# Kernel tuning notes

Measured on AMD Instinct MI355X. Metric: run time of the kernel, lower is better.

The kernel has to match this reference:

```python
import jax, jax.numpy as jnp
import numpy as np

B = 1048576
IN, H = 16, 12


def _xavier(key, shape):
    fan_out, fan_in = shape
    lim = jnp.sqrt(6.0 / (fan_in + fan_out))
    return jax.random.uniform(key, shape, jnp.float32, -lim, lim)


def _lstm_cell_zero_state(x, W_ih, b_ih, b_hh):
    # PyTorch LSTMCell with h0=c0=0: h0 @ W_hh.T == 0, so W_hh drops out of
    # the forward math (its gradient is exactly zero); b_hh still contributes.
    gates = x @ W_ih.T + b_ih + b_hh          # [B, 4H]
    i, f, g, o = jnp.split(gates, 4, axis=-1)  # PyTorch gate order: i,f,g,o
    c = jax.nn.sigmoid(i) * jnp.tanh(g)        # f*c0 == 0
    h = jax.nn.sigmoid(o) * jnp.tanh(c)
    return h


def setup_inputs() -> dict:
    key = jax.random.key(0)
    ks = jax.random.split(key, 9)
    x = jax.random.normal(ks[0], (B, IN), jnp.float32)
    d = {"x": x}
    specs = [("1", IN), ("2", H), ("m", H), ("d", H)]
    for idx, (tag, in_dim) in enumerate(specs):
        kw, kb = jax.random.split(ks[idx + 1])
        d[f"W_ih{tag}"] = _xavier(kw, (4 * H, in_dim))
        kb1, kb2 = jax.random.split(kb)
        lim = 1.0 / np.sqrt(H)
        d[f"b_ih{tag}"] = jax.random.uniform(kb1, (4 * H,), jnp.float32, -lim, lim)
        d[f"b_hh{tag}"] = jax.random.uniform(kb2, (4 * H,), jnp.float32, -lim, lim)
    return d


def reference(x, W_ih1, b_ih1, b_hh1, W_ih2, b_ih2, b_hh2,
              W_ihm, b_ihm, b_hhm, W_ihd, b_ihd, b_hhd):
    h1 = jax.nn.relu(_lstm_cell_zero_state(x, W_ih1, b_ih1, b_hh1))
    h2 = jax.nn.selu(_lstm_cell_zero_state(h1, W_ih2, b_ih2, b_hh2))
    m = jnp.tanh(_lstm_cell_zero_state(h2, W_ihm, b_ihm, b_hhm))
    dv = jnp.tanh(_lstm_cell_zero_state(h2, W_ihd, b_ihd, b_hhd))
    return jnp.concatenate([m, dv], axis=0)  # [2B, H]
```

## Files before the change

### kernel.cpp

```cpp
#include <hip/hip_runtime.h>

#define L2E 1.4426950408889634f

typedef float v2f __attribute__((ext_vector_type(2)));

__device__ __forceinline__ v2f exp2v(v2f a) {
    v2f r; r.x = __builtin_amdgcn_exp2f(a.x); r.y = __builtin_amdgcn_exp2f(a.y); return r;
}
__device__ __forceinline__ v2f rcpv(v2f a) {
    v2f r; r.x = __builtin_amdgcn_rcpf(a.x); r.y = __builtin_amdgcn_rcpf(a.y); return r;
}
__device__ __forceinline__ v2f fmav(v2f a, v2f b, v2f c) {
    return __builtin_elementwise_fma(a, b, c);
}
__device__ __forceinline__ v2f tanh_pade(v2f xv) {
    v2f x2 = xv * xv;
    v2f num = xv * (945.0f + x2 * (105.0f + x2));
    v2f den = 945.0f + x2 * (420.0f + 15.0f * x2);
    return num * rcpv(den);
}

__global__ void prep_kernel(
    const float* __restrict__ W1, const float* __restrict__ bi1, const float* __restrict__ bh1,
    const float* __restrict__ W2, const float* __restrict__ bi2, const float* __restrict__ bh2,
    const float* __restrict__ Wm, const float* __restrict__ bim, const float* __restrict__ bhm,
    const float* __restrict__ Wd, const float* __restrict__ bid, const float* __restrict__ bhd,
    float* __restrict__ ws)
{
    const float* Ws[4]  = {W1, W2, Wm, Wd};
    const float* bis[4] = {bi1, bi2, bim, bid};
    const float* bhs[4] = {bh1, bh2, bhm, bhd};
    const int   Ks[4]   = {16, 12, 12, 12};
    const int   wOff[4] = {0, 576, 1008, 1440};
    const int   goff[3] = {0, 24, 36};
    const float gsc[3]  = {-L2E, -2.0f * L2E, -L2E};

    int tid = threadIdx.x + blockIdx.x * blockDim.x;
    int nth = blockDim.x * gridDim.x;
    for (int c = 0; c < 4; ++c) {
        int K = Ks[c];
        int n = 3 * 6 * K * 2;
        for (int t = tid; t < n; t += nth) {
            int e  = t & 1;
            int u  = t >> 1;
            int k  = u % K;
            int g  = (u / K) % 3;
            int jp = u / (3 * K);
            int row = goff[g] + 2 * jp + e;
            ws[wOff[c] + t] = gsc[g] * Ws[c][row * K + k];
        }
        for (int t = tid; t < 36; t += nth) {
            int e  = t & 1;
            int u  = t >> 1;
            int g  = u % 3;
            int jp = u / 3;
            int row = goff[g] + 2 * jp + e;
            ws[1872 + c * 36 + t] = gsc[g] * (bis[c][row] + bhs[c][row]);
        }
    }
}

template <int K>
__device__ __forceinline__ void cell_core(const float* __restrict__ wsW,
                                          const float* __restrict__ wsB,
                                          const v2f* xs, v2f h[6])
{
#pragma unroll
    for (int jp = 0; jp < 6; ++jp) {
        const v2f* w  = reinterpret_cast<const v2f*>(wsW) + jp * 3 * K;
        const v2f* bp = reinterpret_cast<const v2f*>(wsB) + jp * 3;
        v2f ai = bp[0], ag = bp[1], ao = bp[2];
#pragma unroll
        for (int k = 0; k < K; ++k) {
            ai = fmav(w[k],         xs[k], ai);
            ag = fmav(w[K + k],     xs[k], ag);
            ao = fmav(w[2 * K + k], xs[k], ao);
        }
        v2f ei = exp2v(ai);
        v2f tg = exp2v(ag);
        v2f eo = exp2v(ao);
        v2f r_ig = rcpv((1.0f + ei) * (1.0f + tg));
        v2f c    = (1.0f - tg) * r_ig;
        v2f c2   = c * c;
        v2f num  = c * (945.0f + c2 * (105.0f + c2));
        v2f den  = 945.0f + c2 * (420.0f + 15.0f * c2);
        v2f r_o  = rcpv((1.0f + eo) * den);
        h[jp]    = num * r_o;
    }
}

__global__ __launch_bounds__(256) void dynnet_kernel(
    const float* __restrict__ x, const float* __restrict__ ws,
    float* __restrict__ out, int nrows)
{
    int row = blockIdx.x * blockDim.x + threadIdx.x;
    if (row >= nrows) return;

    const float* W1 = ws;
    const float* W2 = ws + 576;
    const float* Wm = ws + 1008;
    const float* Wd = ws + 1440;
    const float* B1 = ws + 1872;
    const float* B2 = ws + 1908;
    const float* Bm = ws + 1944;
    const float* Bd = ws + 1980;

    v2f xs[16];
    const float4* xv = reinterpret_cast<const float4*>(x + (size_t)row * 16);
#pragma unroll
    for (int i = 0; i < 4; ++i) {
        float4 v = xv[i];
        xs[4 * i + 0].x = xs[4 * i + 0].y = v.x;
        xs[4 * i + 1].x = xs[4 * i + 1].y = v.y;
        xs[4 * i + 2].x = xs[4 * i + 2].y = v.z;
        xs[4 * i + 3].x = xs[4 * i + 3].y = v.w;
    }

    v2f h[6];

    cell_core<16>(W1, B1, xs, h);
    v2f h1s[12];
#pragma unroll
    for (int jp = 0; jp < 6; ++jp) {
        v2f r = __builtin_elementwise_max(h[jp], (v2f)0.0f);
        h1s[2 * jp + 0].x = h1s[2 * jp + 0].y = r.x;
        h1s[2 * jp + 1].x = h1s[2 * jp + 1].y = r.y;
    }

    cell_core<12>(W2, B2, h1s, h);
    v2f h2s[12];
#pragma unroll
    for (int jp = 0; jp < 6; ++jp) {
        v2f v  = h[jp];
        v2f ev = exp2v(v * L2E);
        v2f ng = fmav(ev, (v2f)1.7580993408473766f, (v2f)(-1.7580993408473766f));
        v2f ps = v * 1.0507009873554805f;
        v2f s;
        s.x = v.x > 0.0f ? ps.x : ng.x;
        s.y = v.y > 0.0f ? ps.y : ng.y;
        h2s[2 * jp + 0].x = h2s[2 * jp + 0].y = s.x;
        h2s[2 * jp + 1].x = h2s[2 * jp + 1].y = s.y;
    }

    v2f hm[6], hd[6];
    cell_core<12>(Wm, Bm, h2s, hm);
    cell_core<12>(Wd, Bd, h2s, hd);

    float mo[12], dvo[12];
#pragma unroll
    for (int jp = 0; jp < 6; ++jp) {
        v2f tm = tanh_pade(hm[jp]);
        v2f td = tanh_pade(hd[jp]);
        mo[2 * jp]  = tm.x; mo[2 * jp + 1]  = tm.y;
        dvo[2 * jp] = td.x; dvo[2 * jp + 1] = td.y;
    }

    float4* om = reinterpret_cast<float4*>(out + (size_t)row * 12);
    float4* od = reinterpret_cast<float4*>(out + ((size_t)nrows + row) * 12);
    om[0] = make_float4(mo[0], mo[1], mo[2],  mo[3]);
    om[1] = make_float4(mo[4], mo[5], mo[6],  mo[7]);
    om[2] = make_float4(mo[8], mo[9], mo[10], mo[11]);
    od[0] = make_float4(dvo[0], dvo[1], dvo[2],  dvo[3]);
    od[1] = make_float4(dvo[4], dvo[5], dvo[6],  dvo[7]);
    od[2] = make_float4(dvo[8], dvo[9], dvo[10], dvo[11]);
}

extern "C" void kernel_launch(void* const* d_in, const int* in_sizes, int n_in,
                              void* d_out, int out_size, void* d_ws, size_t ws_size,
                              hipStream_t stream) {
    const float* x    = (const float*)d_in[0];
    const float* Wih1 = (const float*)d_in[1];
    const float* bih1 = (const float*)d_in[2];
    const float* bhh1 = (const float*)d_in[3];
    const float* Wih2 = (const float*)d_in[4];
    const float* bih2 = (const float*)d_in[5];
    const float* bhh2 = (const float*)d_in[6];
    const float* Wihm = (const float*)d_in[7];
    const float* bihm = (const float*)d_in[8];
    const float* bhhm = (const float*)d_in[9];
    const float* Wihd = (const float*)d_in[10];
    const float* bihd = (const float*)d_in[11];
    const float* bhhd = (const float*)d_in[12];
    float* out = (float*)d_out;
    float* ws  = (float*)d_ws;

    prep_kernel<<<4, 256, 0, stream>>>(Wih1, bih1, bhh1, Wih2, bih2, bhh2,
                                       Wihm, bihm, bhhm, Wihd, bihd, bhhd, ws);

    int nrows = in_sizes[0] / 16;
    int block = 256;
    int grid  = (nrows + block - 1) / block;
    dynnet_kernel<<<grid, block, 0, stream>>>(x, ws, out, nrows);
}
```

Measured before the change: 213.5 us.

## Pack two rows per thread into v2f lanes instead of two hidden units

Changes the packed-math layout so each thread processes two batch rows (t and t+half) in the two lanes of v2f, with weights duplicated across lanes, rather than pairing adjacent hidden units of one row. This drops the per-layer broadcast/shuffle of activations into both lanes and halves the thread count. The cost is twice the register state per thread, which may lower occupancy, and an odd row count would leave the last row unprocessed.

New measurement: 231.1 us. 1.08x slower.

```diff
diff --git a/kernel.cpp b/kernel.cpp
--- a/kernel.cpp
+++ b/kernel.cpp
@@ -30,139 +30,132 @@
     const float* Ws[4]  = {W1, W2, Wm, Wd};
     const float* bis[4] = {bi1, bi2, bim, bid};
     const float* bhs[4] = {bh1, bh2, bhm, bhd};
-    const int   Ks[4]   = {16, 12, 12, 12};
-    const int   wOff[4] = {0, 576, 1008, 1440};
     const int   goff[3] = {0, 24, 36};
     const float gsc[3]  = {-L2E, -2.0f * L2E, -L2E};
 
-    int tid = threadIdx.x + blockIdx.x * blockDim.x;
-    int nth = blockDim.x * gridDim.x;
-    for (int c = 0; c < 4; ++c) {
-        int K = Ks[c];
-        int n = 3 * 6 * K * 2;
-        for (int t = tid; t < n; t += nth) {
-            int e  = t & 1;
-            int u  = t >> 1;
-            int k  = u % K;
-            int g  = (u / K) % 3;
-            int jp = u / (3 * K);
-            int row = goff[g] + 2 * jp + e;
-            ws[wOff[c] + t] = gsc[g] * Ws[c][row * K + k];
-        }
-        for (int t = tid; t < 36; t += nth) {
-            int e  = t & 1;
-            int u  = t >> 1;
-            int g  = u % 3;
-            int jp = u / 3;
-            int row = goff[g] + 2 * jp + e;
-            ws[1872 + c * 36 + t] = gsc[g] * (bis[c][row] + bhs[c][row]);
-        }
+    int t = blockIdx.x * blockDim.x + threadIdx.x;
+    if (t < 1872) {
+        int c, base, K;
+        if (t < 576)       { c = 0; base = 0;    K = 16; }
+        else if (t < 1008) { c = 1; base = 576;  K = 12; }
+        else if (t < 1440) { c = 2; base = 1008; K = 12; }
+        else               { c = 3; base = 1440; K = 12; }
+        int pi = t - base;
+        int k  = pi % K;
+        int g  = (pi / K) % 3;
+        int j  = pi / (3 * K);
+        float v = gsc[g] * Ws[c][(goff[g] + j) * K + k];
+        ws[2 * t] = v; ws[2 * t + 1] = v;
+    } else if (t < 2016) {
+        int u = t - 1872;
+        int c = u / 36;
+        int v0 = u % 36;
+        int j = v0 / 3, g = v0 % 3;
+        float v = gsc[g] * (bis[c][goff[g] + j] + bhs[c][goff[g] + j]);
+        ws[2 * t] = v; ws[2 * t + 1] = v;
     }
 }
 
 template <int K>
-__device__ __forceinline__ void cell_core(const float* __restrict__ wsW,
-                                          const float* __restrict__ wsB,
-                                          const v2f* xs, v2f h[6])
+__device__ __forceinline__ void cell_core(const v2f* __restrict__ w,
+                                          const v2f* __restrict__ b,
+                                          const v2f* xs, v2f h[12])
 {
 #pragma unroll
-    for (int jp = 0; jp < 6; ++jp) {
-        const v2f* w  = reinterpret_cast<const v2f*>(wsW) + jp * 3 * K;
-        const v2f* bp = reinterpret_cast<const v2f*>(wsB) + jp * 3;
-        v2f ai = bp[0], ag = bp[1], ao = bp[2];
+    for (int j = 0; j < 12; ++j) {
+        const v2f* wj = w + j * 3 * K;
+        v2f ai = b[j * 3 + 0], ag = b[j * 3 + 1], ao = b[j * 3 + 2];
 #pragma unroll
         for (int k = 0; k < K; ++k) {
-            ai = fmav(w[k],         xs[k], ai);
-            ag = fmav(w[K + k],     xs[k], ag);
-            ao = fmav(w[2 * K + k], xs[k], ao);
+            ai = fmav(wj[k],         xs[k], ai);
+            ag = fmav(wj[K + k],     xs[k], ag);
+            ao = fmav(wj[2 * K + k], xs[k], ao);
         }
         v2f ei = exp2v(ai);
         v2f tg = exp2v(ag);
         v2f eo = exp2v(ao);
-        v2f r_ig = rcpv((1.0f + ei) * (1.0f + tg));
-        v2f c    = (1.0f - tg) * r_ig;
-        v2f c2   = c * c;
-        v2f num  = c * (945.0f + c2 * (105.0f + c2));
-        v2f den  = 945.0f + c2 * (420.0f + 15.0f * c2);
-        v2f r_o  = rcpv((1.0f + eo) * den);
-        h[jp]    = num * r_o;
+        v2f rig = rcpv((1.0f + ei) * (1.0f + tg));
+        v2f c   = (1.0f - tg) * rig;
+        v2f c2  = c * c;
+        v2f num = c * (945.0f + c2 * (105.0f + c2));
+        v2f den = 945.0f + c2 * (420.0f + 15.0f * c2);
+        v2f ro  = rcpv((1.0f + eo) * den);
+        h[j]    = num * ro;
     }
 }
 
 __global__ __launch_bounds__(256) void dynnet_kernel(
-    const float* __restrict__ x, const float* __restrict__ ws,
+    const float* __restrict__ x, const float* __restrict__ wsf,
     float* __restrict__ out, int nrows)
 {
-    int row = blockIdx.x * blockDim.x + threadIdx.x;
-    if (row >= nrows) return;
+    int t = blockIdx.x * blockDim.x + threadIdx.x;
+    int half = nrows >> 1;
+    if (t >= half) return;
 
-    const float* W1 = ws;
-    const float* W2 = ws + 576;
-    const float* Wm = ws + 1008;
-    const float* Wd = ws + 1440;
-    const float* B1 = ws + 1872;
-    const float* B2 = ws + 1908;
-    const float* Bm = ws + 1944;
-    const float* Bd = ws + 1980;
+    const v2f* wv = (const v2f*)wsf;
+    const v2f* W1 = wv;        const v2f* W2 = wv + 576;
+    const v2f* Wm = wv + 1008; const v2f* Wd = wv + 1440;
+    const v2f* B1 = wv + 1872; const v2f* B2 = wv + 1908;
+    const v2f* Bm = wv + 1944; const v2f* Bd = wv + 1980;
 
     v2f xs[16];
-    const float4* xv = reinterpret_cast<const float4*>(x + (size_t)row * 16);
+    const float4* xa = (const float4*)(x + (size_t)t * 16);
+    const float4* xb = (const float4*)(x + (size_t)(t + half) * 16);
 #pragma unroll
     for (int i = 0; i < 4; ++i) {
-        float4 v = xv[i];
-        xs[4 * i + 0].x = xs[4 * i + 0].y = v.x;
-        xs[4 * i + 1].x = xs[4 * i + 1].y = v.y;
-        xs[4 * i + 2].x = xs[4 * i + 2].y = v.z;
-        xs[4 * i + 3].x = xs[4 * i + 3].y = v.w;
+        float4 a = xa[i], b = xb[i];
+        xs[4 * i + 0] = (v2f){a.x, b.x};
+        xs[4 * i + 1] = (v2f){a.y, b.y};
+        xs[4 * i + 2] = (v2f){a.z, b.z};
+        xs[4 * i + 3] = (v2f){a.w, b.w};
     }
 
-    v2f h[6];
+    v2f h[12], g[12];
 
     cell_core<16>(W1, B1, xs, h);
-    v2f h1s[12];
 #pragma unroll
-    for (int jp = 0; jp < 6; ++jp) {
-        v2f r = __builtin_elementwise_max(h[jp], (v2f)0.0f);
-        h1s[2 * jp + 0].x = h1s[2 * jp + 0].y = r.x;
-        h1s[2 * jp + 1].x = h1s[2 * jp + 1].y = r.y;
-    }
+    for (int j = 0; j < 12; ++j) h[j] = __builtin_elementwise_max(h[j], (v2f)0.0f);
 
-    cell_core<12>(W2, B2, h1s, h);
-    v2f h2s[12];
+    cell_core<12>(W2, B2, h, g);
 #pragma unroll
-    for (int jp = 0; jp < 6; ++jp) {
-        v2f v  = h[jp];
+    for (int j = 0; j < 12; ++j) {
+        v2f v  = g[j];
         v2f ev = exp2v(v * L2E);
         v2f ng = fmav(ev, (v2f)1.7580993408473766f, (v2f)(-1.7580993408473766f));
         v2f ps = v * 1.0507009873554805f;
         v2f s;
         s.x = v.x > 0.0f ? ps.x : ng.x;
         s.y = v.y > 0.0f ? ps.y : ng.y;
-        h2s[2 * jp + 0].x = h2s[2 * jp + 0].y = s.x;
-        h2s[2 * jp + 1].x = h2s[2 * jp + 1].y = s.y;
+        g[j] = s;
     }
 
-    v2f hm[6], hd[6];
-    cell_core<12>(Wm, Bm, h2s, hm);
-    cell_core<12>(Wd, Bd, h2s, hd);
+    v2f hm[12], hd[12];
+    cell_core<12>(Wm, Bm, g, hm);
+    cell_core<12>(Wd, Bd, g, hd);
 
-    float mo[12], dvo[12];
+    v2f tm[12], td[12];
 #pragma unroll
-    for (int jp = 0; jp < 6; ++jp) {
-        v2f tm = tanh_pade(hm[jp]);
-        v2f td = tanh_pade(hd[jp]);
-        mo[2 * jp]  = tm.x; mo[2 * jp + 1]  = tm.y;
-        dvo[2 * jp] = td.x; dvo[2 * jp + 1] = td.y;
+    for (int j = 0; j < 12; ++j) {
+        tm[j] = tanh_pade(hm[j]);
+        td[j] = tanh_pade(hd[j]);
     }
 
-    float4* om = reinterpret_cast<float4*>(out + (size_t)row * 12);
-    float4* od = reinterpret_cast<float4*>(out + ((size_t)nrows + row) * 12);
-    om[0] = make_float4(mo[0], mo[1], mo[2],  mo[3]);
-    om[1] = make_float4(mo[4], mo[5], mo[6],  mo[7]);
-    om[2] = make_float4(mo[8], mo[9], mo[10], mo[11]);
-    od[0] = make_float4(dvo[0], dvo[1], dvo[2],  dvo[3]);
-    od[1] = make_float4(dvo[4], dvo[5], dvo[6],  dvo[7]);
-    od[2] = make_float4(dvo[8], dvo[9], dvo[10], dvo[11]);
+    float4* om0 = (float4*)(out + (size_t)t * 12);
+    float4* om1 = (float4*)(out + (size_t)(t + half) * 12);
+    float4* od0 = (float4*)(out + ((size_t)nrows + t) * 12);
+    float4* od1 = (float4*)(out + ((size_t)nrows + t + half) * 12);
+    om0[0] = make_float4(tm[0].x, tm[1].x, tm[2].x,  tm[3].x);
+    om0[1] = make_float4(tm[4].x, tm[5].x, tm[6].x,  tm[7].x);
+    om0[2] = make_float4(tm[8].x, tm[9].x, tm[10].x, tm[11].x);
+    om1[0] = make_float4(tm[0].y, tm[1].y, tm[2].y,  tm[3].y);
+    om1[1] = make_float4(tm[4].y, tm[5].y, tm[6].y,  tm[7].y);
+    om1[2] = make_float4(tm[8].y, tm[9].y, tm[10].y, tm[11].y);
+    od0[0] = make_float4(td[0].x, td[1].x, td[2].x,  td[3].x);
+    od0[1] = make_float4(td[4].x, td[5].x, td[6].x,  td[7].x);
+    od0[2] = make_float4(td[8].x, td[9].x, td[10].x, td[11].x);
+    od1[0] = make_float4(td[0].y, td[1].y, td[2].y,  td[3].y);
+    od1[1] = make_float4(td[4].y, td[5].y, td[6].y,  td[7].y);
+    od1[2] = make_float4(td[8].y, td[9].y, td[10].y, td[11].y);
 }
 
 extern "C" void kernel_launch(void* const* d_in, const int* in_sizes, int n_in,
@@ -184,11 +177,12 @@
     float* out = (float*)d_out;
     float* ws  = (float*)d_ws;
 
-    prep_kernel<<<4, 256, 0, stream>>>(Wih1, bih1, bhh1, Wih2, bih2, bhh2,
+    prep_kernel<<<8, 256, 0, stream>>>(Wih1, bih1, bhh1, Wih2, bih2, bhh2,
                                        Wihm, bihm, bhhm, Wihd, bihd, bhhd, ws);
 
     int nrows = in_sizes[0] / 16;
+    int half  = nrows >> 1;
     int block = 256;
-    int grid  = (nrows + block - 1) / block;
+    int grid  = (half + block - 1) / block;
     dynnet_kernel<<<grid, block, 0, stream>>>(x, ws, out, nrows);
 }
```
